# Kernel tuning notes

Hardware: AMD Instinct MI355X
Metric: run time of the kernel (lower is better)

The kernel has to match this reference:

```python
import jax, jax.numpy as jnp
import numpy as np

B, C, H, W, D = 4, 64, 64, 192, 24


def setup_inputs() -> dict:
    key = jax.random.key(0)
    ks = jax.random.split(key, 8)
    x = jax.random.normal(ks[0], (B, C, H, W), dtype=jnp.float32)
    y = jax.random.normal(ks[1], (B, C, H, W), dtype=jnp.float32)
    # disparity coordinate samples: pixel x-coordinates in [0, W-1]
    d1 = jax.random.uniform(ks[2], (B, D, H, W), dtype=jnp.float32) * (W - 1.0)
    d2 = jax.random.uniform(ks[3], (B, D, H, W), dtype=jnp.float32) * (W - 1.0)
    s = 1.0 / np.sqrt(C)
    qw = jax.random.normal(ks[4], (C, C), dtype=jnp.float32) * s
    qb = jax.random.normal(ks[5], (C,), dtype=jnp.float32) * 0.01
    kw = jax.random.normal(ks[6], (C, C), dtype=jnp.float32) * s
    kb = jax.random.normal(ks[7], (C,), dtype=jnp.float32) * 0.01
    return {"x": x, "y": y, "disp_range_samples1": d1, "disp_range_samples2": d2,
            "ndisp": D, "qw": qw, "qb": qb, "kw": kw, "kb": kb}


def _conv1x1(x, w, b):
    return jnp.einsum('oi,bihw->bohw', w, x) + b[None, :, None, None]


def _cost_volume(Q, K, disp_x):
    """mean_c( Q * grid_sample(K, bilinear, zeros, align_corners=False) ).
    Q,K: [B,C,H,W]; disp_x: [B,D,H,W] pixel x-coords. Returns [B,D,H,W]."""
    b, c, h, w = K.shape
    # torch grid_sample(align_corners=False) unnormalization of
    # coords = pix/((dim-1)/2)-1  ->  pix*dim/(dim-1) - 0.5
    xs = disp_x * (w / (w - 1.0)) - 0.5                      # [B,D,H,W]
    ys_row = jnp.arange(h, dtype=xs.dtype) * (h / (h - 1.0)) - 0.5
    ys = jnp.broadcast_to(ys_row[None, None, :, None], xs.shape)
    x0 = jnp.floor(xs)
    y0 = jnp.floor(ys)
    tx = xs - x0
    ty = ys - y0
    x0i = x0.astype(jnp.int32)
    y0i = y0.astype(jnp.int32)

    def corner(dy, dx, wgt):
        yi = y0i + dy
        xi = x0i + dx
        valid = ((yi >= 0) & (yi < h) & (xi >= 0) & (xi < w)).astype(Q.dtype)
        yc = jnp.clip(yi, 0, h - 1)
        xc = jnp.clip(xi, 0, w - 1)
        # per-batch gather: [C,H,W] indexed by [D,H,W] -> [C,D,H,W]
        g = jax.vmap(lambda im, yy, xx: im[:, yy, xx])(K, yc, xc)  # [B,C,D,H,W]
        return jnp.einsum('bchw,bcdhw->bdhw', Q, g * (wgt * valid)[:, None])

    cost = (corner(0, 0, (1.0 - ty) * (1.0 - tx)) +
            corner(0, 1, (1.0 - ty) * tx) +
            corner(1, 0, ty * (1.0 - tx)) +
            corner(1, 1, ty * tx))
    return cost / c


def reference(x, y, disp_range_samples1, disp_range_samples2, ndisp, qw, qb, kw, kb):
    assert ndisp == disp_range_samples1.shape[1]
    Q1 = _conv1x1(x, qw, qb)
    K1 = _conv1x1(y, kw, kb)
    cost1 = _cost_volume(Q1, K1, disp_range_samples1)
    Q2 = _conv1x1(y, qw, qb)
    K2 = _conv1x1(x, kw, kb)
    cost2 = _cost_volume(Q2, K2, disp_range_samples2)
    return (cost1, cost2)
```

## Files before the change

### kernel.cpp

```cpp
#include <hip/hip_runtime.h>
#include <stdint.h>

#define BB 4
#define CC 64
#define HH 64
#define WW 192
#define DD 24
#define HWQ (HH * WW)
#define PIX (BB * HWQ)

typedef __attribute__((ext_vector_type(8))) short short8;
typedef __attribute__((ext_vector_type(4))) float floatx4;

__device__ __forceinline__ float bf1(uint16_t u) {
    union { uint32_t i; float f; } c; c.i = ((uint32_t)u) << 16; return c.f;
}
__device__ __forceinline__ uint16_t f2bf(float f) {
    union { float f; uint32_t i; } c; c.f = f;
    uint32_t u = c.i;
    return (uint16_t)((u + 0x7fffu + ((u >> 16) & 1u)) >> 16);
}

#define A_SHORTS ((size_t)2 * PIX * CC)
#define S_F32OFF 4240

__global__ __launch_bounds__(64) void prep_kernel(
    const float* __restrict__ qw, const float* __restrict__ qb,
    const float* __restrict__ kw, const float* __restrict__ kb,
    float* __restrict__ fws) {
    const int bid = blockIdx.x;
    const int j   = threadIdx.x;
    if (bid < 64) {
        float acc = 0.f;
        for (int c = 0; c < CC; c++)
            acc = fmaf(qw[c * CC + bid], kw[c * CC + j], acc);
        fws[bid * 64 + j] = acc;
    } else if (bid == 64) {
        float bt = 0.f;
        for (int c = 0; c < CC; c++) bt = fmaf(qb[c], kw[c * CC + j], bt);
        fws[4096 + j] = bt;
        if (j == 0) {
            float g = 0.f;
            for (int c = 0; c < CC; c++) g = fmaf(qb[c], kb[c], g);
            fws[4224] = g;
        }
    } else {
        float al = 0.f;
        for (int c = 0; c < CC; c++) al = fmaf(qw[c * CC + j], kb[c], al);
        fws[4160 + j] = al;
    }
}

__global__ __launch_bounds__(256) void convA_kernel(
    const float* __restrict__ x, const float* __restrict__ y,
    const float* __restrict__ fws, uint16_t* __restrict__ A,
    uint16_t* __restrict__ Ybf) {
    const int v = blockIdx.y;
    const float* src = v ? y : x;
    float* s = const_cast<float*>(fws) + S_F32OFF;

    __shared__ float wt[64][64];
    __shared__ float bs[64], al[64];
    __shared__ float gm;
    const int tid = threadIdx.y * 64 + threadIdx.x;
    for (int idx = tid; idx < 4096; idx += 256) wt[idx >> 6][idx & 63] = fws[idx];
    if (tid < 64) { bs[tid] = fws[4096 + tid]; al[tid] = fws[4160 + tid]; }
    if (tid == 64) gm = fws[4224];
    __syncthreads();

    const int pix0 = blockIdx.x * 256 + threadIdx.x * 4;
    const int b    = pix0 / HWQ;
    const int hw0  = pix0 - b * HWQ;
    const int j0   = threadIdx.y * 16;

    float acc[4][16];
#pragma unroll
    for (int p = 0; p < 4; p++)
#pragma unroll
        for (int k = 0; k < 16; k++) acc[p][k] = bs[j0 + k];
    float sac[4] = {gm, gm, gm, gm};

    const float*    sp   = src + (size_t)b * CC * HWQ + hw0;
    uint16_t*       Ymir = Ybf + (size_t)v * PIX * CC + (size_t)b * CC * HWQ + hw0;
#pragma unroll 4
    for (int i = 0; i < 64; i++) {
        float4 raw = *reinterpret_cast<const float4*>(sp + (size_t)i * HWQ);
        if ((i & 3) == threadIdx.y) {
            uint2 pv;
            pv.x = (uint32_t)f2bf(raw.x) | ((uint32_t)f2bf(raw.y) << 16);
            pv.y = (uint32_t)f2bf(raw.z) | ((uint32_t)f2bf(raw.w) << 16);
            *reinterpret_cast<uint2*>(Ymir + (size_t)i * HWQ) = pv;
        }
        const float* wr = &wt[i][j0];
        const float av = al[i];
        sac[0] = fmaf(raw.x, av, sac[0]);
        sac[1] = fmaf(raw.y, av, sac[1]);
        sac[2] = fmaf(raw.z, av, sac[2]);
        sac[3] = fmaf(raw.w, av, sac[3]);
#pragma unroll
        for (int k = 0; k < 16; k++) {
            float wv = wr[k];
            acc[0][k] = fmaf(raw.x, wv, acc[0][k]);
            acc[1][k] = fmaf(raw.y, wv, acc[1][k]);
            acc[2][k] = fmaf(raw.z, wv, acc[2][k]);
            acc[3][k] = fmaf(raw.w, wv, acc[3][k]);
        }
    }

    uint16_t* dstv = A + (size_t)v * PIX * CC;
#pragma unroll
    for (int p = 0; p < 4; p++) {
        uint32_t pk[8];
#pragma unroll
        for (int k = 0; k < 8; k++)
            pk[k] = (uint32_t)f2bf(acc[p][2 * k]) | ((uint32_t)f2bf(acc[p][2 * k + 1]) << 16);
        uint16_t* dp = dstv + (size_t)(pix0 + p) * CC + j0;
        uint4 lo; lo.x = pk[0]; lo.y = pk[1]; lo.z = pk[2]; lo.w = pk[3];
        uint4 hi; hi.x = pk[4]; hi.y = pk[5]; hi.z = pk[6]; hi.w = pk[7];
        *reinterpret_cast<uint4*>(dp)     = lo;
        *reinterpret_cast<uint4*>(dp + 8) = hi;
    }
    if (threadIdx.y == 0) {
        float4 sv; sv.x = sac[0]; sv.y = sac[1]; sv.z = sac[2]; sv.w = sac[3];
        *reinterpret_cast<float4*>(s + (size_t)v * PIX + pix0) = sv;
    }
}

__global__ __launch_bounds__(1024) void cost_kernel(
    const float* __restrict__ disp1, const float* __restrict__ disp2,
    const uint16_t* __restrict__ A, const uint16_t* __restrict__ Ybf,
    const float* __restrict__ fws, float* __restrict__ out) {
    const int h = blockIdx.x;
    const int b = blockIdx.y;
    const int v = blockIdx.z;

    const int       tsel = v ? 0 : 1;
    const float*    disp = v ? disp2 : disp1;
    const uint16_t* Ab   = A + ((size_t)v * PIX + (size_t)b * HWQ + h * WW) * CC;
    const float*    sb   = fws + S_F32OFF + (size_t)v * PIX + (size_t)b * HWQ + h * WW;

    const float ys  = (float)h * (float)(64.0 / 63.0) - 0.5f;
    const float y0f = floorf(ys);
    const float ty  = ys - y0f;
    const int   y0  = (int)y0f;
    const int   y1  = y0 + 1;
    const float vy0 = (y0 >= 0 && y0 < HH) ? 1.f : 0.f;
    const float vy1 = (y1 >= 0 && y1 < HH) ? 1.f : 0.f;
    const int   y0c = min(max(y0, 0), HH - 1);
    const int   y1c = min(max(y1, 0), HH - 1);
    const float ey0 = (1.f - ty) * vy0;
    const float ey1 = ty * vy1;
    const float eysum = ey0 + ey1;

    __shared__ uint16_t Yc[192 * 68];
    __shared__ uint16_t Pt[96 * 196];

    const int tid  = threadIdx.x;
    const int wave = tid >> 6;
    const int lane = tid & 63;
    const int lq   = lane >> 4;
    const int ln   = lane & 63 & 0xF;

    const uint16_t* Yb0 = Ybf + (size_t)tsel * PIX * CC + (size_t)b * CC * HWQ + y0c * WW;
    const uint16_t* Yb1 = Ybf + (size_t)tsel * PIX * CC + (size_t)b * CC * HWQ + y1c * WW;
#pragma unroll
    for (int k = 0; k < 3; k++) {
        const int cg = wave;
        const int xx = k * 64 + lane;
        uint32_t pk[2];
#pragma unroll
        for (int half = 0; half < 2; half++) {
            uint32_t pv = 0;
#pragma unroll
            for (int j = 0; j < 2; j++) {
                const int c = cg * 4 + half * 2 + j;
                const float v0 = bf1(Yb0[(size_t)c * HWQ + xx]);
                const float v1 = bf1(Yb1[(size_t)c * HWQ + xx]);
                const float cb = fmaf(ey1, v1, ey0 * v0);
                pv |= ((uint32_t)f2bf(cb)) << (16 * j);
            }
            pk[half] = pv;
        }
        *reinterpret_cast<uint2*>(&Yc[xx * 68 + cg * 4]) = *reinterpret_cast<uint2*>(pk);
    }
    __syncthreads();

    const float cx = (float)(192.0 / 191.0);
    const float inv_c = 1.f / 64.f;

    for (int half = 0; half < 2; half++) {
        if (wave < 12) {
            const int mcl = wave >> 1;
            const uint16_t* ar = Ab + (size_t)(half * 96 + mcl * 16 + ln) * CC + lq * 8;
            short8 a0 = *reinterpret_cast<const short8*>(ar);
            short8 a1 = *reinterpret_cast<const short8*>(ar + 32);
#pragma unroll
            for (int i = 0; i < 6; i++) {
                const int nt = (wave & 1) * 6 + i;
                const int Rb = nt * 16;
                const uint16_t* yrow = &Yc[(Rb + ln) * 68 + lq * 8];
                short8 b0, b1;
                *reinterpret_cast<uint2*>(&b0)       = *reinterpret_cast<const uint2*>(yrow);
                *(reinterpret_cast<uint2*>(&b0) + 1) = *reinterpret_cast<const uint2*>(yrow + 4);
                *reinterpret_cast<uint2*>(&b1)       = *reinterpret_cast<const uint2*>(yrow + 32);
                *(reinterpret_cast<uint2*>(&b1) + 1) = *reinterpret_cast<const uint2*>(yrow + 36);
                floatx4 acc = {0.f, 0.f, 0.f, 0.f};
                acc = __builtin_amdgcn_mfma_f32_16x16x32_bf16(a0, b0, acc, 0, 0, 0);
                acc = __builtin_amdgcn_mfma_f32_16x16x32_bf16(a1, b1, acc, 0, 0, 0);
                const int pcol = Rb + ln;
                const int wl   = mcl * 16 + lq * 4;
                Pt[(wl + 0) * 196 + pcol] = f2bf(acc[0]);
                Pt[(wl + 1) * 196 + pcol] = f2bf(acc[1]);
                Pt[(wl + 2) * 196 + pcol] = f2bf(acc[2]);
                Pt[(wl + 3) * 196 + pcol] = f2bf(acc[3]);
            }
        }
        __syncthreads();

        for (int o = tid; o < 96 * DD; o += 1024) {
            const int wl = o % 96;
            const int d  = o / 96;
            const int w  = half * 96 + wl;
            const float dsv = disp[((size_t)(b * DD + d) * HH + h) * WW + w];
            const float xs  = dsv * cx - 0.5f;
            const float x0f = floorf(xs);
            const float tx  = xs - x0f;
            const int   x0  = (int)x0f;
            const int   x1  = x0 + 1;
            const float vx0 = (x0 >= 0 && x0 < WW) ? 1.f : 0.f;
            const float vx1 = (x1 >= 0 && x1 < WW) ? 1.f : 0.f;
            const int   x0c = min(max(x0, 0), WW - 1);
            const int   x1c = min(max(x1, 0), WW - 1);
            const float wx0 = (1.f - tx) * vx0;
            const float wx1 = tx * vx1;
            const float pc0 = bf1(Pt[wl * 196 + x0c]);
            const float pc1 = bf1(Pt[wl * 196 + x1c]);
            const float res = wx0 * pc0 + wx1 * pc1 + sb[w] * (eysum * (wx0 + wx1));
            out[(((size_t)(v * BB + b) * DD + d) * HH + h) * WW + w] = res * inv_c;
        }
        if (half == 0) __syncthreads();
    }
}

extern "C" void kernel_launch(void* const* d_in, const int* in_sizes, int n_in,
                              void* d_out, int out_size, void* d_ws, size_t ws_size,
                              hipStream_t stream) {
    const float* x  = (const float*)d_in[0];
    const float* y  = (const float*)d_in[1];
    const float* d1 = (const float*)d_in[2];
    const float* d2 = (const float*)d_in[3];
    const float* qw = (const float*)d_in[5];
    const float* qb = (const float*)d_in[6];
    const float* kw = (const float*)d_in[7];
    const float* kb = (const float*)d_in[8];

    uint16_t* A   = (uint16_t*)d_ws;
    uint16_t* Ybf = (uint16_t*)d_ws + A_SHORTS;
    float*    fws = (float*)((uint16_t*)d_ws + 2 * A_SHORTS);
    float*    out = (float*)d_out;

    prep_kernel<<<dim3(66), dim3(64), 0, stream>>>(qw, qb, kw, kb, fws);
    convA_kernel<<<dim3(PIX / 256, 2), dim3(64, 4), 0, stream>>>(x, y, fws, A, Ybf);
    cost_kernel<<<dim3(HH, BB, 2), dim3(1024), 0, stream>>>(d1, d2, A, Ybf, fws, out);
}
```

Before: 127.1 us.

## Fold weight-product prep into convA, widen convA blocks, prefetch cost-kernel operands

Removes the separate prep kernel launch: each convA block now recomputes the combined qw^T·kw matrix and bias vectors itself, and the block grows to 512 threads with each thread holding 8 output channels instead of 16. In cost_kernel, the A fragments for both halves plus the disparity and s values are loaded up front, before the Y staging and sync, so their global latency overlaps other work. This trades one kernel launch and lower register pressure against redundant per-block weight computation (about 256K FMAs per block) and more live registers in the cost kernel.

```diff
diff --git a/kernel.cpp b/kernel.cpp
--- a/kernel.cpp
+++ b/kernel.cpp
@@ -24,60 +24,63 @@
 #define A_SHORTS ((size_t)2 * PIX * CC)
 #define S_F32OFF 4240
 
-__global__ __launch_bounds__(64) void prep_kernel(
+__global__ __launch_bounds__(512) void convA_kernel(
+    const float* __restrict__ x, const float* __restrict__ y,
     const float* __restrict__ qw, const float* __restrict__ qb,
     const float* __restrict__ kw, const float* __restrict__ kb,
-    float* __restrict__ fws) {
-    const int bid = blockIdx.x;
-    const int j   = threadIdx.x;
-    if (bid < 64) {
-        float acc = 0.f;
-        for (int c = 0; c < CC; c++)
-            acc = fmaf(qw[c * CC + bid], kw[c * CC + j], acc);
-        fws[bid * 64 + j] = acc;
-    } else if (bid == 64) {
-        float bt = 0.f;
-        for (int c = 0; c < CC; c++) bt = fmaf(qb[c], kw[c * CC + j], bt);
-        fws[4096 + j] = bt;
-        if (j == 0) {
-            float g = 0.f;
-            for (int c = 0; c < CC; c++) g = fmaf(qb[c], kb[c], g);
-            fws[4224] = g;
-        }
-    } else {
-        float al = 0.f;
-        for (int c = 0; c < CC; c++) al = fmaf(qw[c * CC + j], kb[c], al);
-        fws[4160 + j] = al;
-    }
-}
-
-__global__ __launch_bounds__(256) void convA_kernel(
-    const float* __restrict__ x, const float* __restrict__ y,
-    const float* __restrict__ fws, uint16_t* __restrict__ A,
+    float* __restrict__ fws, uint16_t* __restrict__ A,
     uint16_t* __restrict__ Ybf) {
     const int v = blockIdx.y;
     const float* src = v ? y : x;
-    float* s = const_cast<float*>(fws) + S_F32OFF;
+    float* s = fws + S_F32OFF;
 
     __shared__ float wt[64][64];
     __shared__ float bs[64], al[64];
     __shared__ float gm;
-    const int tid = threadIdx.y * 64 + threadIdx.x;
-    for (int idx = tid; idx < 4096; idx += 256) wt[idx >> 6][idx & 63] = fws[idx];
-    if (tid < 64) { bs[tid] = fws[4096 + tid]; al[tid] = fws[4160 + tid]; }
-    if (tid == 64) gm = fws[4224];
+
+    const int tx  = threadIdx.x;
+    const int ty  = threadIdx.y;
+    const int tid = ty * 64 + tx;
+
+    {
+        float ga[8];
+#pragma unroll
+        for (int k = 0; k < 8; k++) ga[k] = 0.f;
+        for (int c = 0; c < 64; c++) {
+            const float kwv = kw[c * CC + tx];
+#pragma unroll
+            for (int k = 0; k < 8; k++)
+                ga[k] = fmaf(qw[c * CC + (k * 8 + ty)], kwv, ga[k]);
+        }
+#pragma unroll
+        for (int k = 0; k < 8; k++) wt[k * 8 + ty][tx] = ga[k];
+    }
+    if (tid < 64) {
+        float bt = 0.f;
+        for (int c = 0; c < 64; c++) bt = fmaf(qb[c], kw[c * CC + tid], bt);
+        bs[tid] = bt;
+    } else if (tid < 128) {
+        const int i = tid - 64;
+        float a = 0.f;
+        for (int c = 0; c < 64; c++) a = fmaf(qw[c * CC + i], kb[c], a);
+        al[i] = a;
+    } else if (tid == 128) {
+        float g = 0.f;
+        for (int c = 0; c < 64; c++) g = fmaf(qb[c], kb[c], g);
+        gm = g;
+    }
     __syncthreads();
 
-    const int pix0 = blockIdx.x * 256 + threadIdx.x * 4;
+    const int pix0 = blockIdx.x * 256 + tx * 4;
     const int b    = pix0 / HWQ;
     const int hw0  = pix0 - b * HWQ;
-    const int j0   = threadIdx.y * 16;
-
-    float acc[4][16];
+    const int j0   = ty * 8;
+
+    float acc[4][8];
 #pragma unroll
     for (int p = 0; p < 4; p++)
 #pragma unroll
-        for (int k = 0; k < 16; k++) acc[p][k] = bs[j0 + k];
+        for (int k = 0; k < 8; k++) acc[p][k] = bs[j0 + k];
     float sac[4] = {gm, gm, gm, gm};
 
     const float*    sp   = src + (size_t)b * CC * HWQ + hw0;
@@ -85,20 +88,22 @@
 #pragma unroll 4
     for (int i = 0; i < 64; i++) {
         float4 raw = *reinterpret_cast<const float4*>(sp + (size_t)i * HWQ);
-        if ((i & 3) == threadIdx.y) {
+        if ((i & 7) == ty) {
             uint2 pv;
             pv.x = (uint32_t)f2bf(raw.x) | ((uint32_t)f2bf(raw.y) << 16);
             pv.y = (uint32_t)f2bf(raw.z) | ((uint32_t)f2bf(raw.w) << 16);
             *reinterpret_cast<uint2*>(Ymir + (size_t)i * HWQ) = pv;
         }
         const float* wr = &wt[i][j0];
-        const float av = al[i];
-        sac[0] = fmaf(raw.x, av, sac[0]);
-        sac[1] = fmaf(raw.y, av, sac[1]);
-        sac[2] = fmaf(raw.z, av, sac[2]);
-        sac[3] = fmaf(raw.w, av, sac[3]);
-#pragma unroll
-        for (int k = 0; k < 16; k++) {
+        if (ty == 0) {
+            const float av = al[i];
+            sac[0] = fmaf(raw.x, av, sac[0]);
+            sac[1] = fmaf(raw.y, av, sac[1]);
+            sac[2] = fmaf(raw.z, av, sac[2]);
+            sac[3] = fmaf(raw.w, av, sac[3]);
+        }
+#pragma unroll
+        for (int k = 0; k < 8; k++) {
             float wv = wr[k];
             acc[0][k] = fmaf(raw.x, wv, acc[0][k]);
             acc[1][k] = fmaf(raw.y, wv, acc[1][k]);
@@ -110,17 +115,15 @@
     uint16_t* dstv = A + (size_t)v * PIX * CC;
 #pragma unroll
     for (int p = 0; p < 4; p++) {
-        uint32_t pk[8];
-#pragma unroll
-        for (int k = 0; k < 8; k++)
+        uint32_t pk[4];
+#pragma unroll
+        for (int k = 0; k < 4; k++)
             pk[k] = (uint32_t)f2bf(acc[p][2 * k]) | ((uint32_t)f2bf(acc[p][2 * k + 1]) << 16);
         uint16_t* dp = dstv + (size_t)(pix0 + p) * CC + j0;
-        uint4 lo; lo.x = pk[0]; lo.y = pk[1]; lo.z = pk[2]; lo.w = pk[3];
-        uint4 hi; hi.x = pk[4]; hi.y = pk[5]; hi.z = pk[6]; hi.w = pk[7];
-        *reinterpret_cast<uint4*>(dp)     = lo;
-        *reinterpret_cast<uint4*>(dp + 8) = hi;
-    }
-    if (threadIdx.y == 0) {
+        uint4 w4; w4.x = pk[0]; w4.y = pk[1]; w4.z = pk[2]; w4.w = pk[3];
+        *reinterpret_cast<uint4*>(dp) = w4;
+    }
+    if (ty == 0) {
         float4 sv; sv.x = sac[0]; sv.y = sac[1]; sv.z = sac[2]; sv.w = sac[3];
         *reinterpret_cast<float4*>(s + (size_t)v * PIX + pix0) = sv;
     }
@@ -159,7 +162,38 @@
     const int wave = tid >> 6;
     const int lane = tid & 63;
     const int lq   = lane >> 4;
-    const int ln   = lane & 63 & 0xF;
+    const int ln   = lane & 15;
+
+    short8 a0f[2], a1f[2];
+    if (wave < 12) {
+        const int mcl = wave >> 1;
+#pragma unroll
+        for (int hf = 0; hf < 2; hf++) {
+            const uint16_t* ar = Ab + (size_t)(hf * 96 + mcl * 16 + ln) * CC + lq * 8;
+            a0f[hf] = *reinterpret_cast<const short8*>(ar);
+            a1f[hf] = *reinterpret_cast<const short8*>(ar + 32);
+        }
+    }
+
+    float dpre[2][3], spre[2][3];
+#pragma unroll
+    for (int hf = 0; hf < 2; hf++)
+#pragma unroll
+        for (int q = 0; q < 3; q++) { dpre[hf][q] = 0.f; spre[hf][q] = 0.f; }
+#pragma unroll
+    for (int hf = 0; hf < 2; hf++) {
+#pragma unroll
+        for (int q = 0; q < 3; q++) {
+            const int o = tid + q * 1024;
+            if (o < 96 * DD) {
+                const int wl = o % 96;
+                const int d  = o / 96;
+                const int w  = hf * 96 + wl;
+                dpre[hf][q] = disp[((size_t)(b * DD + d) * HH + h) * WW + w];
+                spre[hf][q] = sb[w];
+            }
+        }
+    }
 
     const uint16_t* Yb0 = Ybf + (size_t)tsel * PIX * CC + (size_t)b * CC * HWQ + y0c * WW;
     const uint16_t* Yb1 = Ybf + (size_t)tsel * PIX * CC + (size_t)b * CC * HWQ + y1c * WW;
@@ -188,12 +222,12 @@
     const float cx = (float)(192.0 / 191.0);
     const float inv_c = 1.f / 64.f;
 
+#pragma unroll
     for (int half = 0; half < 2; half++) {
         if (wave < 12) {
             const int mcl = wave >> 1;
-            const uint16_t* ar = Ab + (size_t)(half * 96 + mcl * 16 + ln) * CC + lq * 8;
-            short8 a0 = *reinterpret_cast<const short8*>(ar);
-            short8 a1 = *reinterpret_cast<const short8*>(ar + 32);
+            const short8 a0 = a0f[half];
+            const short8 a1 = a1f[half];
 #pragma unroll
             for (int i = 0; i < 6; i++) {
                 const int nt = (wave & 1) * 6 + i;
@@ -217,26 +251,30 @@
         }
         __syncthreads();
 
-        for (int o = tid; o < 96 * DD; o += 1024) {
-            const int wl = o % 96;
-            const int d  = o / 96;
-            const int w  = half * 96 + wl;
-            const float dsv = disp[((size_t)(b * DD + d) * HH + h) * WW + w];
-            const float xs  = dsv * cx - 0.5f;
-            const float x0f = floorf(xs);
-            const float tx  = xs - x0f;
-            const int   x0  = (int)x0f;
-            const int   x1  = x0 + 1;
-            const float vx0 = (x0 >= 0 && x0 < WW) ? 1.f : 0.f;
-            const float vx1 = (x1 >= 0 && x1 < WW) ? 1.f : 0.f;
-            const int   x0c = min(max(x0, 0), WW - 1);
-            const int   x1c = min(max(x1, 0), WW - 1);
-            const float wx0 = (1.f - tx) * vx0;
-            const float wx1 = tx * vx1;
-            const float pc0 = bf1(Pt[wl * 196 + x0c]);
-            const float pc1 = bf1(Pt[wl * 196 + x1c]);
-            const float res = wx0 * pc0 + wx1 * pc1 + sb[w] * (eysum * (wx0 + wx1));
-            out[(((size_t)(v * BB + b) * DD + d) * HH + h) * WW + w] = res * inv_c;
+#pragma unroll
+        for (int q = 0; q < 3; q++) {
+            const int o = tid + q * 1024;
+            if (o < 96 * DD) {
+                const int wl = o % 96;
+                const int d  = o / 96;
+                const int w  = half * 96 + wl;
+                const float dsv = dpre[half][q];
+                const float xs  = dsv * cx - 0.5f;
+                const float x0f = floorf(xs);
+                const float tx  = xs - x0f;
+                const int   x0  = (int)x0f;
+                const int   x1  = x0 + 1;
+                const float vx0 = (x0 >= 0 && x0 < WW) ? 1.f : 0.f;
+                const float vx1 = (x1 >= 0 && x1 < WW) ? 1.f : 0.f;
+                const int   x0c = min(max(x0, 0), WW - 1);
+                const int   x1c = min(max(x1, 0), WW - 1);
+                const float wx0 = (1.f - tx) * vx0;
+                const float wx1 = tx * vx1;
+                const float pc0 = bf1(Pt[wl * 196 + x0c]);
+                const float pc1 = bf1(Pt[wl * 196 + x1c]);
+                const float res = wx0 * pc0 + wx1 * pc1 + spre[half][q] * (eysum * (wx0 + wx1));
+                out[(((size_t)(v * BB + b) * DD + d) * HH + h) * WW + w] = res * inv_c;
+            }
         }
         if (half == 0) __syncthreads();
     }
@@ -259,7 +297,7 @@
     float*    fws = (float*)((uint16_t*)d_ws + 2 * A_SHORTS);
     float*    out = (float*)d_out;
 
-    prep_kernel<<<dim3(66), dim3(64), 0, stream>>>(qw, qb, kw, kb, fws);
-    convA_kernel<<<dim3(PIX / 256, 2), dim3(64, 4), 0, stream>>>(x, y, fws, A, Ybf);
+    convA_kernel<<<dim3(PIX / 256, 2), dim3(64, 8), 0, stream>>>(
+        x, y, qw, qb, kw, kb, fws, A, Ybf);
     cost_kernel<<<dim3(HH, BB, 2), dim3(1024), 0, stream>>>(d1, d2, A, Ybf, fws, out);
 }
```

Result: slower. 145.2 us (+14.2%).

## Drop bf16 mirror of inputs; read fp32 rows directly in cost kernel

Applied to the files above, without the earlier changes.

The conv kernel no longer writes a bf16 copy of x/y to workspace. The cost kernel instead reads the two needed fp32 rows straight from the original inputs and rounds them to bf16 on the fly, so results match the old path. This removes a full-size workspace write and shrinks the workspace, at the cost of doubling the bytes read per row in the cost kernel. It also hoists the A-fragment loads for both halves to the kernel start so they overlap the row staging, and adds unroll pragmas to the small prep loops.

```diff
diff --git a/kernel.cpp b/kernel.cpp
--- a/kernel.cpp
+++ b/kernel.cpp
@@ -32,20 +32,24 @@
     const int j   = threadIdx.x;
     if (bid < 64) {
         float acc = 0.f;
+#pragma unroll 8
         for (int c = 0; c < CC; c++)
             acc = fmaf(qw[c * CC + bid], kw[c * CC + j], acc);
         fws[bid * 64 + j] = acc;
     } else if (bid == 64) {
         float bt = 0.f;
+#pragma unroll 8
         for (int c = 0; c < CC; c++) bt = fmaf(qb[c], kw[c * CC + j], bt);
         fws[4096 + j] = bt;
         if (j == 0) {
             float g = 0.f;
+#pragma unroll 8
             for (int c = 0; c < CC; c++) g = fmaf(qb[c], kb[c], g);
             fws[4224] = g;
         }
     } else {
         float al = 0.f;
+#pragma unroll 8
         for (int c = 0; c < CC; c++) al = fmaf(qw[c * CC + j], kb[c], al);
         fws[4160 + j] = al;
     }
@@ -53,11 +57,10 @@
 
 __global__ __launch_bounds__(256) void convA_kernel(
     const float* __restrict__ x, const float* __restrict__ y,
-    const float* __restrict__ fws, uint16_t* __restrict__ A,
-    uint16_t* __restrict__ Ybf) {
+    float* __restrict__ fws, uint16_t* __restrict__ A) {
     const int v = blockIdx.y;
     const float* src = v ? y : x;
-    float* s = const_cast<float*>(fws) + S_F32OFF;
+    float* s = fws + S_F32OFF;
 
     __shared__ float wt[64][64];
     __shared__ float bs[64], al[64];
@@ -80,17 +83,10 @@
         for (int k = 0; k < 16; k++) acc[p][k] = bs[j0 + k];
     float sac[4] = {gm, gm, gm, gm};
 
-    const float*    sp   = src + (size_t)b * CC * HWQ + hw0;
-    uint16_t*       Ymir = Ybf + (size_t)v * PIX * CC + (size_t)b * CC * HWQ + hw0;
+    const float* sp = src + (size_t)b * CC * HWQ + hw0;
 #pragma unroll 4
     for (int i = 0; i < 64; i++) {
         float4 raw = *reinterpret_cast<const float4*>(sp + (size_t)i * HWQ);
-        if ((i & 3) == threadIdx.y) {
-            uint2 pv;
-            pv.x = (uint32_t)f2bf(raw.x) | ((uint32_t)f2bf(raw.y) << 16);
-            pv.y = (uint32_t)f2bf(raw.z) | ((uint32_t)f2bf(raw.w) << 16);
-            *reinterpret_cast<uint2*>(Ymir + (size_t)i * HWQ) = pv;
-        }
         const float* wr = &wt[i][j0];
         const float av = al[i];
         sac[0] = fmaf(raw.x, av, sac[0]);
@@ -127,14 +123,15 @@
 }
 
 __global__ __launch_bounds__(1024) void cost_kernel(
+    const float* __restrict__ x, const float* __restrict__ y,
     const float* __restrict__ disp1, const float* __restrict__ disp2,
-    const uint16_t* __restrict__ A, const uint16_t* __restrict__ Ybf,
-    const float* __restrict__ fws, float* __restrict__ out) {
+    const uint16_t* __restrict__ A, const float* __restrict__ fws,
+    float* __restrict__ out) {
     const int h = blockIdx.x;
     const int b = blockIdx.y;
     const int v = blockIdx.z;
 
-    const int       tsel = v ? 0 : 1;
+    const float*    ksrc = (v ? x : y) + (size_t)b * CC * HWQ;
     const float*    disp = v ? disp2 : disp1;
     const uint16_t* Ab   = A + ((size_t)v * PIX + (size_t)b * HWQ + h * WW) * CC;
     const float*    sb   = fws + S_F32OFF + (size_t)v * PIX + (size_t)b * HWQ + h * WW;
@@ -159,10 +156,21 @@
     const int wave = tid >> 6;
     const int lane = tid & 63;
     const int lq   = lane >> 4;
-    const int ln   = lane & 63 & 0xF;
-
-    const uint16_t* Yb0 = Ybf + (size_t)tsel * PIX * CC + (size_t)b * CC * HWQ + y0c * WW;
-    const uint16_t* Yb1 = Ybf + (size_t)tsel * PIX * CC + (size_t)b * CC * HWQ + y1c * WW;
+    const int ln   = lane & 15;
+
+    short8 a0f[2], a1f[2];
+    if (wave < 12) {
+        const int mcl = wave >> 1;
+#pragma unroll
+        for (int hf = 0; hf < 2; hf++) {
+            const uint16_t* ar = Ab + (size_t)(hf * 96 + mcl * 16 + ln) * CC + lq * 8;
+            a0f[hf] = *reinterpret_cast<const short8*>(ar);
+            a1f[hf] = *reinterpret_cast<const short8*>(ar + 32);
+        }
+    }
+
+    const float* Yb0 = ksrc + (size_t)y0c * WW;
+    const float* Yb1 = ksrc + (size_t)y1c * WW;
 #pragma unroll
     for (int k = 0; k < 3; k++) {
         const int cg = wave;
@@ -174,8 +182,8 @@
 #pragma unroll
             for (int j = 0; j < 2; j++) {
                 const int c = cg * 4 + half * 2 + j;
-                const float v0 = bf1(Yb0[(size_t)c * HWQ + xx]);
-                const float v1 = bf1(Yb1[(size_t)c * HWQ + xx]);
+                const float v0 = bf1(f2bf(Yb0[(size_t)c * HWQ + xx]));
+                const float v1 = bf1(f2bf(Yb1[(size_t)c * HWQ + xx]));
                 const float cb = fmaf(ey1, v1, ey0 * v0);
                 pv |= ((uint32_t)f2bf(cb)) << (16 * j);
             }
@@ -188,12 +196,12 @@
     const float cx = (float)(192.0 / 191.0);
     const float inv_c = 1.f / 64.f;
 
+#pragma unroll
     for (int half = 0; half < 2; half++) {
         if (wave < 12) {
             const int mcl = wave >> 1;
-            const uint16_t* ar = Ab + (size_t)(half * 96 + mcl * 16 + ln) * CC + lq * 8;
-            short8 a0 = *reinterpret_cast<const short8*>(ar);
-            short8 a1 = *reinterpret_cast<const short8*>(ar + 32);
+            const short8 a0 = a0f[half];
+            const short8 a1 = a1f[half];
 #pragma unroll
             for (int i = 0; i < 6; i++) {
                 const int nt = (wave & 1) * 6 + i;
@@ -255,11 +263,10 @@
     const float* kb = (const float*)d_in[8];
 
     uint16_t* A   = (uint16_t*)d_ws;
-    uint16_t* Ybf = (uint16_t*)d_ws + A_SHORTS;
-    float*    fws = (float*)((uint16_t*)d_ws + 2 * A_SHORTS);
+    float*    fws = (float*)((uint16_t*)d_ws + A_SHORTS);
     float*    out = (float*)d_out;
 
     prep_kernel<<<dim3(66), dim3(64), 0, stream>>>(qw, qb, kw, kb, fws);
-    convA_kernel<<<dim3(PIX / 256, 2), dim3(64, 4), 0, stream>>>(x, y, fws, A, Ybf);
-    cost_kernel<<<dim3(HH, BB, 2), dim3(1024), 0, stream>>>(d1, d2, A, Ybf, fws, out);
-}
+    convA_kernel<<<dim3(PIX / 256, 2), dim3(64, 4), 0, stream>>>(x, y, fws, A);
+    cost_kernel<<<dim3(HH, BB, 2), dim3(1024), 0, stream>>>(x, y, d1, d2, A, fws, out);
+}
```

Measured after the change: 130.7 us. 2.8% more time.
